# Kernel tuning notes

Measured on AMD Instinct MI355X. Metric: run time of the kernel, lower is better.

Reference implementation:

```python
import jax, jax.numpy as jnp
import numpy as np

B, C, N, H = 4, 256, 4096, 4
DK = C // H


def _proj(x, w, b):
    # Conv1d with kernel size 1 == per-point linear: [B,C,N] x [O,C] -> [B,O,N]
    return jnp.einsum('oc,bcn->bon', w, x) + b[None, :, None]


def setup_inputs() -> dict:
    key = jax.random.key(0)
    ks = jax.random.split(key, 9)
    s = 1.0 / np.sqrt(C)
    return {
        'x': jax.random.normal(ks[0], (B, C, N), jnp.float32),
        'wq': jax.random.normal(ks[1], (C, C), jnp.float32) * s,
        'bq': jax.random.normal(ks[2], (C,), jnp.float32) * 0.01,
        'wk': jax.random.normal(ks[3], (C, C), jnp.float32) * s,
        'bk': jax.random.normal(ks[4], (C,), jnp.float32) * 0.01,
        'wv': jax.random.normal(ks[5], (C, C), jnp.float32) * s,
        'bv': jax.random.normal(ks[6], (C,), jnp.float32) * 0.01,
        'wp': jax.random.normal(ks[7], (C, C), jnp.float32) * s,
        'bp': jax.random.normal(ks[8], (C,), jnp.float32) * 0.01,
    }


def reference(x, wq, bq, wk, bk, wv, bv, wp, bp):
    b, c, n = x.shape
    q = _proj(x, wq, bq).reshape(b, H, DK, n)
    k = _proj(x, wk, bk).reshape(b, H, DK, n)
    v = _proj(x, wv, bv).reshape(b, H, DK, n)
    scale = 1.0 / jnp.sqrt(jnp.asarray(DK, x.dtype))
    # scores over point pairs: [B,H,N,N]
    scores = jnp.einsum('bhdn,bhdm->bhnm', q, k) * scale
    attn = jax.nn.softmax(scores, axis=-1)
    out = jnp.einsum('bhnm,bhdm->bhdn', attn, v)  # [B,H,DK,N]
    out = out.reshape(b, c, n)
    out = _proj(out, wp, bp)
    return out + x
```

## Files before the change

### kernel.cpp

```cpp
#include <hip/hip_runtime.h>


#define BDIM 4
#define CDIM 256
#define NDIM 4096
#define HDIM 4
#define DKDIM 64
#define NQ   (BDIM * HDIM * NDIM)
#define QSCALE 0.18033688011112042f

typedef __bf16 bf16x8 __attribute__((ext_vector_type(8)));
typedef float f32x4 __attribute__((ext_vector_type(4)));
typedef short s16x4 __attribute__((ext_vector_type(4)));
typedef unsigned short u16;
typedef unsigned int u32;

__device__ __forceinline__ u16 f2bf(float f) {
  union { __bf16 h; u16 s; } u; u.h = (__bf16)f; return u.s;
}
__device__ __forceinline__ float bf2f(u16 v) {
  union { u32 u; float f; } x; x.u = (u32)v << 16; return x.f;
}
__device__ __forceinline__ u32 pk2(float a, float b) {
  return (u32)f2bf(a) | ((u32)f2bf(b) << 16);
}

__global__ __launch_bounds__(256) void xt_kernel(
    const float* __restrict__ x, u16* __restrict__ xT)
{
  const int b = blockIdx.z, c0 = blockIdx.y * 64, n0 = blockIdx.x * 64;
  __shared__ __align__(16) float T[64][68];
  const int t = threadIdx.x;
  {
    const int cr = t >> 4, nc = (t & 15) * 4;
    #pragma unroll
    for (int ci = 0; ci < 4; ++ci) {
      const float4 v = *(const float4*)&x[((size_t)(b * CDIM + c0 + cr + ci * 16)) * NDIM + n0 + nc];
      *(float4*)&T[cr + ci * 16][nc] = v;
    }
  }
  __syncthreads();
  {
    const int n = t >> 2, g = t & 3;
    union { u16 u[16]; uint4 v[2]; } pk;
    #pragma unroll
    for (int u_ = 0; u_ < 16; ++u_) pk.u[u_] = f2bf(T[g * 16 + u_][n]);
    uint4* dst = (uint4*)&xT[((size_t)(b * NDIM + n0 + n)) * CDIM + c0 + g * 16];
    dst[0] = pk.v[0]; dst[1] = pk.v[1];
  }
}

__global__ __launch_bounds__(256, 4) void qkv_kernel(
    const u16* __restrict__ xT,
    const float* __restrict__ wq, const float* __restrict__ bq,
    const float* __restrict__ wk, const float* __restrict__ bk,
    const float* __restrict__ wv, const float* __restrict__ bv,
    u16* __restrict__ qT, u16* __restrict__ kT, u16* __restrict__ vB)
{
  const int b = blockIdx.z;
  const int p = blockIdx.y >> 2;
  const int o0 = (blockIdx.y & 3) * 64;
  const int n0 = blockIdx.x * 64;
  const float* wsel = (p == 0) ? wq : (p == 1) ? wk : wv;
  const float* bsel = (p == 0) ? bq : (p == 1) ? bk : bv;
  const float wscale = (p == 0) ? QSCALE : 1.0f;

  __shared__ __align__(16) u16 XTs[64][40];
  __shared__ __align__(16) u16 Ws[64][40];
  const int t = threadIdx.x, lane = t & 63, w = t >> 6;
  const int qd = lane >> 4, lm = lane & 15;
  const int sr = t >> 2, sg = (t & 3) * 8;

  const u16* xsrc = xT + ((size_t)(b * NDIM + n0 + sr)) * CDIM + sg;
  const float* wsrc = wsel + (size_t)(o0 + sr) * CDIM + sg;

  f32x4 acc[4];
  #pragma unroll
  for (int nt = 0; nt < 4; ++nt) acc[nt] = (f32x4){0.f, 0.f, 0.f, 0.f};

  for (int cs = 0; cs < 8; ++cs) {
    __syncthreads();
    *(uint4*)&XTs[sr][sg] = *(const uint4*)(xsrc + cs * 32);
    {
      const float4 w0 = *(const float4*)(wsrc + cs * 32);
      const float4 w1 = *(const float4*)(wsrc + cs * 32 + 4);
      union { u32 p[4]; uint4 v; } pw;
      pw.p[0] = pk2(w0.x * wscale, w0.y * wscale);
      pw.p[1] = pk2(w0.z * wscale, w0.w * wscale);
      pw.p[2] = pk2(w1.x * wscale, w1.y * wscale);
      pw.p[3] = pk2(w1.z * wscale, w1.w * wscale);
      *(uint4*)&Ws[sr][sg] = pw.v;
    }
    __syncthreads();
    bf16x8 xf[4];
    #pragma unroll
    for (int nt = 0; nt < 4; ++nt) xf[nt] = *(const bf16x8*)&XTs[16 * nt + lm][qd * 8];
    const bf16x8 wf = *(const bf16x8*)&Ws[16 * w + lm][qd * 8];
    #pragma unroll
    for (int nt = 0; nt < 4; ++nt) {
      if (p < 2)
        acc[nt] = __builtin_amdgcn_mfma_f32_16x16x32_bf16(xf[nt], wf, acc[nt], 0, 0, 0);
      else
        acc[nt] = __builtin_amdgcn_mfma_f32_16x16x32_bf16(wf, xf[nt], acc[nt], 0, 0, 0);
    }
  }

  if (p < 2) {
    u16* out = (p == 0) ? qT : kT;
    const int og = o0 + 16 * w + lm;
    const float bv2 = bsel[og] * wscale;
    #pragma unroll
    for (int nt = 0; nt < 4; ++nt)
      #pragma unroll
      for (int r = 0; r < 4; ++r) {
        const int n = n0 + 16 * nt + 4 * qd + r;
        out[((size_t)(b * NDIM + n)) * CDIM + og] = f2bf(acc[nt][r] + bv2);
      }
  } else {
    const float4 b4 = *(const float4*)&bsel[o0 + 16 * w + 4 * qd];
    const float bvr[4] = {b4.x, b4.y, b4.z, b4.w};
    #pragma unroll
    for (int nt = 0; nt < 4; ++nt)
      #pragma unroll
      for (int r = 0; r < 4; ++r) {
        const int og = o0 + 16 * w + 4 * qd + r;
        const int n = n0 + 16 * nt + lm;
        vB[((size_t)(b * CDIM + og)) * NDIM + n] = f2bf(acc[nt][r] + bvr[r]);
      }
  }
}

__global__ __launch_bounds__(256, 4) void attn_kernel(
    const u16* __restrict__ qT, const u16* __restrict__ kT,
    const u16* __restrict__ vB, u16* __restrict__ Opart,
    float* __restrict__ Lp)
{
  const int bh = blockIdx.y, b = bh >> 2, h = bh & 3;
  const int n0 = blockIdx.x * 128;
  const int z  = blockIdx.z;
  __shared__ __align__(16) u16 Qt[128][64];
  __shared__ __align__(16) u16 Kt[64][72];
  __shared__ __align__(16) u16 Vt[64][72];

  const int t = threadIdx.x, lane = t & 63, w = t >> 6;
  const int qd = lane >> 4, lm = lane & 15;

  {
    const int r = t >> 1, g = (t & 1) * 32;
    const uint4* src = (const uint4*)&qT[((size_t)(b * NDIM + n0 + r)) * CDIM + h * 64 + g];
    uint4* dst = (uint4*)&Qt[r][g];
    dst[0] = src[0]; dst[1] = src[1]; dst[2] = src[2]; dst[3] = src[3];
  }
  __syncthreads();
  bf16x8 qf[2][2];
  #pragma unroll
  for (int s = 0; s < 2; ++s)
    #pragma unroll
    for (int hh = 0; hh < 2; ++hh)
      qf[s][hh] = *(const bf16x8*)&Qt[16 * (2 * w + s) + lm][32 * hh + qd * 8];

  float l_i[2] = {0.f, 0.f};
  f32x4 oa[2][4];
  #pragma unroll
  for (int s = 0; s < 2; ++s)
    #pragma unroll
    for (int dt = 0; dt < 4; ++dt) oa[s][dt] = (f32x4){0.f, 0.f, 0.f, 0.f};

  const int sr = t >> 2, sg = (t & 3) * 16;
  const u16* kptr = kT + ((size_t)(b * NDIM) + z * 2048 + sr) * CDIM + h * 64 + sg;
  const u16* vptr = vB + ((size_t)(b * CDIM) + h * 64 + sr) * NDIM + z * 2048 + sg;

  for (int it = 0; it < 32; ++it) {
    __syncthreads();
    {
      uint4* kd = (uint4*)&Kt[sr][sg];
      kd[0] = *(const uint4*)(kptr);
      kd[1] = *(const uint4*)(kptr + 8);
      uint4* vd = (uint4*)&Vt[sr][sg];
      vd[0] = *(const uint4*)(vptr);
      vd[1] = *(const uint4*)(vptr + 8);
    }
    kptr += (size_t)64 * CDIM;
    vptr += 64;
    __syncthreads();

    bf16x8 kf[4][2];
    #pragma unroll
    for (int nt = 0; nt < 4; ++nt)
      #pragma unroll
      for (int hh = 0; hh < 2; ++hh)
        kf[nt][hh] = *(const bf16x8*)&Kt[16 * nt + lm][32 * hh + qd * 8];

    float pr[2][4][4];
    #pragma unroll
    for (int s = 0; s < 2; ++s) {
      f32x4 sc[4];
      #pragma unroll
      for (int nt = 0; nt < 4; ++nt) {
        f32x4 zz = (f32x4){0.f, 0.f, 0.f, 0.f};
        zz = __builtin_amdgcn_mfma_f32_16x16x32_bf16(kf[nt][0], qf[s][0], zz, 0, 0, 0);
        zz = __builtin_amdgcn_mfma_f32_16x16x32_bf16(kf[nt][1], qf[s][1], zz, 0, 0, 0);
        sc[nt] = zz;
      }
      float rs = 0.f;
      #pragma unroll
      for (int nt = 0; nt < 4; ++nt)
        #pragma unroll
        for (int r = 0; r < 4; ++r) {
          const float p = __builtin_amdgcn_exp2f(sc[nt][r]);
          pr[s][nt][r] = p;
          rs += p;
        }
      l_i[s] += rs;
    }

    #pragma unroll
    for (int c = 0; c < 4; ++c) {
      s16x4 av[4];
      #pragma unroll
      for (int dt = 0; dt < 4; ++dt)
        av[dt] = *(const s16x4*)&Vt[16 * dt + lm][16 * c + 4 * qd];
      union { u16 u[4]; s16x4 v; } bp0, bp1;
      #pragma unroll
      for (int r = 0; r < 4; ++r) { bp0.u[r] = f2bf(pr[0][c][r]); bp1.u[r] = f2bf(pr[1][c][r]); }
      #pragma unroll
      for (int dt = 0; dt < 4; ++dt) {
        oa[0][dt] = __builtin_amdgcn_mfma_f32_16x16x16bf16_1k(av[dt], bp0.v, oa[0][dt], 0, 0, 0);
        oa[1][dt] = __builtin_amdgcn_mfma_f32_16x16x16bf16_1k(av[dt], bp1.v, oa[1][dt], 0, 0, 0);
      }
    }
  }

  #pragma unroll
  for (int s = 0; s < 2; ++s) {
    l_i[s] += __shfl_xor(l_i[s], 16);
    l_i[s] += __shfl_xor(l_i[s], 32);
  }

  __syncthreads();
  u16 (*Ot)[64] = (u16(*)[64])&Qt[0][0];
  #pragma unroll
  for (int s = 0; s < 2; ++s) {
    const float inv = 1.0f / l_i[s];
    #pragma unroll
    for (int dt = 0; dt < 4; ++dt)
      #pragma unroll
      for (int r = 0; r < 4; ++r)
        Ot[16 * (2 * w + s) + lm][16 * dt + 4 * qd + r] = f2bf(oa[s][dt][r] * inv);
  }
  if (qd == 0) {
    const size_t lbase = ((size_t)z * (BDIM * HDIM) + bh) * NDIM;
    #pragma unroll
    for (int s = 0; s < 2; ++s)
      Lp[lbase + n0 + 16 * (2 * w + s) + lm] = l_i[s];
  }
  __syncthreads();
  {
    const int r = t >> 1, g = (t & 1) * 32;
    u16* dst = Opart + (((size_t)z * (BDIM * HDIM) + bh) * NDIM + n0 + r) * DKDIM + g;
    const uint4* srcp = (const uint4*)&Ot[r][g];
    uint4* d4 = (uint4*)dst;
    d4[0] = srcp[0]; d4[1] = srcp[1]; d4[2] = srcp[2]; d4[3] = srcp[3];
  }
}

__global__ __launch_bounds__(256, 4) void projout_kernel(
    const u16* __restrict__ Opart, const float* __restrict__ Lp,
    const float* __restrict__ wp, const float* __restrict__ bp,
    const float* __restrict__ res, float* __restrict__ out)
{
  const int b = blockIdx.z, o0 = blockIdx.y * 64, n0 = blockIdx.x * 64;
  __shared__ __align__(16) u16 XTs[64][40];
  __shared__ __align__(16) u16 Ws[64][40];
  const int t = threadIdx.x, lane = t & 63, w = t >> 6;
  const int qd = lane >> 4, lm = lane & 15;
  const int sr = t >> 2, sg = (t & 3) * 8;

  float w0h[4], w1h[4];
  #pragma unroll
  for (int hh = 0; hh < 4; ++hh) {
    const size_t i0 = ((size_t)(b * HDIM + hh)) * NDIM + n0 + sr;
    const float l0 = Lp[i0], l1 = Lp[(size_t)NQ + i0];
    const float iv = 1.0f / (l0 + l1);
    w0h[hh] = l0 * iv; w1h[hh] = l1 * iv;
  }

  const float* wsrc = wp + (size_t)(o0 + sr) * CDIM + sg;

  f32x4 acc[4];
  #pragma unroll
  for (int nt = 0; nt < 4; ++nt) acc[nt] = (f32x4){0.f, 0.f, 0.f, 0.f};

  for (int cs = 0; cs < 8; ++cs) {
    const int c0 = cs * 32;
    const int hh = c0 >> 6;
    const int dk = (c0 & 63) + sg;
    __syncthreads();
    {
      const size_t obase = (((size_t)(b * HDIM + hh)) * NDIM + n0 + sr) * DKDIM + dk;
      union { u16 u[8]; uint4 v; } a0, a1, ov;
      a0.v = *(const uint4*)(Opart + obase);
      a1.v = *(const uint4*)(Opart + (size_t)NQ * DKDIM + obase);
      #pragma unroll
      for (int j = 0; j < 8; ++j)
        ov.u[j] = f2bf(w0h[hh] * bf2f(a0.u[j]) + w1h[hh] * bf2f(a1.u[j]));
      *(uint4*)&XTs[sr][sg] = ov.v;
      const float4 wv0 = *(const float4*)(wsrc + c0);
      const float4 wv1 = *(const float4*)(wsrc + c0 + 4);
      union { u32 p[4]; uint4 v; } pw;
      pw.p[0] = pk2(wv0.x, wv0.y);
      pw.p[1] = pk2(wv0.z, wv0.w);
      pw.p[2] = pk2(wv1.x, wv1.y);
      pw.p[3] = pk2(wv1.z, wv1.w);
      *(uint4*)&Ws[sr][sg] = pw.v;
    }
    __syncthreads();
    bf16x8 xf[4];
    #pragma unroll
    for (int nt = 0; nt < 4; ++nt) xf[nt] = *(const bf16x8*)&XTs[16 * nt + lm][qd * 8];
    const bf16x8 wf = *(const bf16x8*)&Ws[16 * w + lm][qd * 8];
    #pragma unroll
    for (int nt = 0; nt < 4; ++nt)
      acc[nt] = __builtin_amdgcn_mfma_f32_16x16x32_bf16(wf, xf[nt], acc[nt], 0, 0, 0);
  }

  const float4 b4 = *(const float4*)&bp[o0 + 16 * w + 4 * qd];
  const float bvr[4] = {b4.x, b4.y, b4.z, b4.w};
  #pragma unroll
  for (int nt = 0; nt < 4; ++nt)
    #pragma unroll
    for (int r = 0; r < 4; ++r) {
      const int og = o0 + 16 * w + 4 * qd + r;
      const int n = n0 + 16 * nt + lm;
      const size_t idx = ((size_t)(b * CDIM + og)) * NDIM + n;
      out[idx] = acc[nt][r] + bvr[r] + res[idx];
    }
}

extern "C" void kernel_launch(void* const* d_in, const int* in_sizes, int n_in,
                              void* d_out, int out_size, void* d_ws, size_t ws_size,
                              hipStream_t stream)
{
  const float* x  = (const float*)d_in[0];
  const float* wq = (const float*)d_in[1];
  const float* bq = (const float*)d_in[2];
  const float* wk = (const float*)d_in[3];
  const float* bk = (const float*)d_in[4];
  const float* wv = (const float*)d_in[5];
  const float* bv = (const float*)d_in[6];
  const float* wp = (const float*)d_in[7];
  const float* bp = (const float*)d_in[8];
  float* out = (float*)d_out;

  const size_t sz = (size_t)BDIM * CDIM * NDIM;
  u16* xTb = (u16*)d_ws;
  u16* qTb = xTb + sz;
  u16* kTb = qTb + sz;
  u16* vBb = kTb + sz;
  u16* Opart = vBb + sz;
  float* Lp = (float*)(Opart + 2 * sz);

  const dim3 blk(256);
  xt_kernel<<<dim3(NDIM / 64, CDIM / 64, BDIM), blk, 0, stream>>>(x, xTb);
  qkv_kernel<<<dim3(NDIM / 64, 12, BDIM), blk, 0, stream>>>(
      xTb, wq, bq, wk, bk, wv, bv, qTb, kTb, vBb);
  attn_kernel<<<dim3(NDIM / 128, BDIM * HDIM, 2), blk, 0, stream>>>(
      qTb, kTb, vBb, Opart, Lp);
  projout_kernel<<<dim3(NDIM / 64, 4, BDIM), blk, 0, stream>>>(
      Opart, Lp, wp, bp, x, out);
}
```

Before: 209.3 us.

## Split attention keys four ways, load Q directly to registers, raise occupancy

```diff
diff --git a/kernel.cpp b/kernel.cpp
--- a/kernel.cpp
+++ b/kernel.cpp
@@ -7,6 +7,8 @@
 #define HDIM 4
 #define DKDIM 64
 #define NQ   (BDIM * HDIM * NDIM)
+#define NSPLIT 4
+#define KPERZ (NDIM / NSPLIT)
 #define QSCALE 0.18033688011112042f
 
 typedef __bf16 bf16x8 __attribute__((ext_vector_type(8)));
@@ -130,7 +132,7 @@
   }
 }
 
-__global__ __launch_bounds__(256, 4) void attn_kernel(
+__global__ __launch_bounds__(256, 8) void attn_kernel(
     const u16* __restrict__ qT, const u16* __restrict__ kT,
     const u16* __restrict__ vB, u16* __restrict__ Opart,
     float* __restrict__ Lp)
@@ -138,26 +140,22 @@
   const int bh = blockIdx.y, b = bh >> 2, h = bh & 3;
   const int n0 = blockIdx.x * 128;
   const int z  = blockIdx.z;
-  __shared__ __align__(16) u16 Qt[128][64];
-  __shared__ __align__(16) u16 Kt[64][72];
-  __shared__ __align__(16) u16 Vt[64][72];
+
+  __shared__ __align__(16) u16 KV[2][64][72];
 
   const int t = threadIdx.x, lane = t & 63, w = t >> 6;
   const int qd = lane >> 4, lm = lane & 15;
 
+  bf16x8 qf[2][2];
   {
-    const int r = t >> 1, g = (t & 1) * 32;
-    const uint4* src = (const uint4*)&qT[((size_t)(b * NDIM + n0 + r)) * CDIM + h * 64 + g];
-    uint4* dst = (uint4*)&Qt[r][g];
-    dst[0] = src[0]; dst[1] = src[1]; dst[2] = src[2]; dst[3] = src[3];
-  }
-  __syncthreads();
-  bf16x8 qf[2][2];
-  #pragma unroll
-  for (int s = 0; s < 2; ++s)
-    #pragma unroll
-    for (int hh = 0; hh < 2; ++hh)
-      qf[s][hh] = *(const bf16x8*)&Qt[16 * (2 * w + s) + lm][32 * hh + qd * 8];
+    const u16* qbase = qT + ((size_t)(b * NDIM) + n0) * CDIM + h * 64;
+    #pragma unroll
+    for (int s = 0; s < 2; ++s)
+      #pragma unroll
+      for (int hh = 0; hh < 2; ++hh)
+        qf[s][hh] = *(const bf16x8*)(qbase +
+            (size_t)(16 * (2 * w + s) + lm) * CDIM + 32 * hh + qd * 8);
+  }
 
   float l_i[2] = {0.f, 0.f};
   f32x4 oa[2][4];
@@ -167,16 +165,16 @@
     for (int dt = 0; dt < 4; ++dt) oa[s][dt] = (f32x4){0.f, 0.f, 0.f, 0.f};
 
   const int sr = t >> 2, sg = (t & 3) * 16;
-  const u16* kptr = kT + ((size_t)(b * NDIM) + z * 2048 + sr) * CDIM + h * 64 + sg;
-  const u16* vptr = vB + ((size_t)(b * CDIM) + h * 64 + sr) * NDIM + z * 2048 + sg;
-
-  for (int it = 0; it < 32; ++it) {
+  const u16* kptr = kT + ((size_t)(b * NDIM) + z * KPERZ + sr) * CDIM + h * 64 + sg;
+  const u16* vptr = vB + ((size_t)(b * CDIM) + h * 64 + sr) * NDIM + z * KPERZ + sg;
+
+  for (int it = 0; it < KPERZ / 64; ++it) {
     __syncthreads();
     {
-      uint4* kd = (uint4*)&Kt[sr][sg];
+      uint4* kd = (uint4*)&KV[0][sr][sg];
       kd[0] = *(const uint4*)(kptr);
       kd[1] = *(const uint4*)(kptr + 8);
-      uint4* vd = (uint4*)&Vt[sr][sg];
+      uint4* vd = (uint4*)&KV[1][sr][sg];
       vd[0] = *(const uint4*)(vptr);
       vd[1] = *(const uint4*)(vptr + 8);
     }
@@ -189,7 +187,7 @@
     for (int nt = 0; nt < 4; ++nt)
       #pragma unroll
       for (int hh = 0; hh < 2; ++hh)
-        kf[nt][hh] = *(const bf16x8*)&Kt[16 * nt + lm][32 * hh + qd * 8];
+        kf[nt][hh] = *(const bf16x8*)&KV[0][16 * nt + lm][32 * hh + qd * 8];
 
     float pr[2][4][4];
     #pragma unroll
@@ -219,7 +217,7 @@
       s16x4 av[4];
       #pragma unroll
       for (int dt = 0; dt < 4; ++dt)
-        av[dt] = *(const s16x4*)&Vt[16 * dt + lm][16 * c + 4 * qd];
+        av[dt] = *(const s16x4*)&KV[1][16 * dt + lm][16 * c + 4 * qd];
       union { u16 u[4]; s16x4 v; } bp0, bp1;
       #pragma unroll
       for (int r = 0; r < 4; ++r) { bp0.u[r] = f2bf(pr[0][c][r]); bp1.u[r] = f2bf(pr[1][c][r]); }
@@ -238,7 +236,7 @@
   }
 
   __syncthreads();
-  u16 (*Ot)[64] = (u16(*)[64])&Qt[0][0];
+  u16 (*Ot)[72] = (u16(*)[72])&KV[0][0][0];
   #pragma unroll
   for (int s = 0; s < 2; ++s) {
     const float inv = 1.0f / l_i[s];
@@ -276,13 +274,16 @@
   const int qd = lane >> 4, lm = lane & 15;
   const int sr = t >> 2, sg = (t & 3) * 8;
 
-  float w0h[4], w1h[4];
+  float wh[4][NSPLIT];
   #pragma unroll
   for (int hh = 0; hh < 4; ++hh) {
     const size_t i0 = ((size_t)(b * HDIM + hh)) * NDIM + n0 + sr;
-    const float l0 = Lp[i0], l1 = Lp[(size_t)NQ + i0];
-    const float iv = 1.0f / (l0 + l1);
-    w0h[hh] = l0 * iv; w1h[hh] = l1 * iv;
+    float l[NSPLIT], tot = 0.f;
+    #pragma unroll
+    for (int zz = 0; zz < NSPLIT; ++zz) { l[zz] = Lp[(size_t)zz * NQ + i0]; tot += l[zz]; }
+    const float iv = 1.0f / tot;
+    #pragma unroll
+    for (int zz = 0; zz < NSPLIT; ++zz) wh[hh][zz] = l[zz] * iv;
   }
 
   const float* wsrc = wp + (size_t)(o0 + sr) * CDIM + sg;
@@ -298,13 +299,19 @@
     __syncthreads();
     {
       const size_t obase = (((size_t)(b * HDIM + hh)) * NDIM + n0 + sr) * DKDIM + dk;
-      union { u16 u[8]; uint4 v; } a0, a1, ov;
-      a0.v = *(const uint4*)(Opart + obase);
-      a1.v = *(const uint4*)(Opart + (size_t)NQ * DKDIM + obase);
-      #pragma unroll
-      for (int j = 0; j < 8; ++j)
-        ov.u[j] = f2bf(w0h[hh] * bf2f(a0.u[j]) + w1h[hh] * bf2f(a1.u[j]));
-      *(uint4*)&XTs[sr][sg] = ov.v;
+      float v[8] = {0.f, 0.f, 0.f, 0.f, 0.f, 0.f, 0.f, 0.f};
+      #pragma unroll
+      for (int zz = 0; zz < NSPLIT; ++zz) {
+        union { u16 u[8]; uint4 q; } a;
+        a.q = *(const uint4*)(Opart + (size_t)zz * NQ * DKDIM + obase);
+        const float wz = wh[hh][zz];
+        #pragma unroll
+        for (int j = 0; j < 8; ++j) v[j] = fmaf(wz, bf2f(a.u[j]), v[j]);
+      }
+      union { u16 u[8]; uint4 q; } ov;
+      #pragma unroll
+      for (int j = 0; j < 8; ++j) ov.u[j] = f2bf(v[j]);
+      *(uint4*)&XTs[sr][sg] = ov.q;
       const float4 wv0 = *(const float4*)(wsrc + c0);
       const float4 wv1 = *(const float4*)(wsrc + c0 + 4);
       union { u32 p[4]; uint4 v; } pw;
@@ -358,13 +365,13 @@
   u16* kTb = qTb + sz;
   u16* vBb = kTb + sz;
   u16* Opart = vBb + sz;
-  float* Lp = (float*)(Opart + 2 * sz);
+  float* Lp = (float*)(Opart + (size_t)NSPLIT * sz);
 
   const dim3 blk(256);
   xt_kernel<<<dim3(NDIM / 64, CDIM / 64, BDIM), blk, 0, stream>>>(x, xTb);
   qkv_kernel<<<dim3(NDIM / 64, 12, BDIM), blk, 0, stream>>>(
       xTb, wq, bq, wk, bk, wv, bv, qTb, kTb, vBb);
-  attn_kernel<<<dim3(NDIM / 128, BDIM * HDIM, 2), blk, 0, stream>>>(
+  attn_kernel<<<dim3(NDIM / 128, BDIM * HDIM, NSPLIT), blk, 0, stream>>>(
       qTb, kTb, vBb, Opart, Lp);
   projout_kernel<<<dim3(NDIM / 64, 4, BDIM), blk, 0, stream>>>(
       Opart, Lp, wp, bp, x, out);
```

After: 827.2 us. +295.1%, slower.
